# Performance work log

Hardware: AMD Instinct MI355X
Metric: run time of the kernel (lower is better)

The kernel has to match this reference:

```python
import jax, jax.numpy as jnp
import numpy as np

B, N, K, H = 8, 4096, 16, 64
EPS_LN = 1e-5
EPS_STD = 1e-5


def _ln(x, g, b):
    m = jnp.mean(x, -1, keepdims=True)
    v = jnp.mean((x - m) ** 2, -1, keepdims=True)
    return (x - m) * jax.lax.rsqrt(v + EPS_LN) * g + b


def _res_block(x, W1, b1, g1, be1, W2, b2, g2, be2):
    h = jax.nn.relu(_ln(x @ W1 + b1, g1, be1))
    return jax.nn.relu(x + _ln(h @ W2 + b2, g2, be2))


def setup_inputs() -> dict:
    key = jax.random.key(0)
    ks = jax.random.split(key, 12)
    def w(k, shape, scale=0.02):
        return (jax.random.normal(k, shape) * scale).astype(jnp.float32)
    h = H
    z = jnp.zeros
    o = jnp.ones
    return dict(
        xyz=jax.random.normal(ks[0], (B, N, 3), jnp.float32),
        x=jax.random.normal(ks[1], (B, N, 3), jnp.float32),
        W_emb=w(ks[2], (3, h)), b_emb=z(h), g_emb=o(h), be_emb=z(h),
        alpha=o(h), beta=z(h),
        W_pre=w(ks[3], (2 * h, 4 * h)), b_pre=z(4 * h), g_pre=o(4 * h), be_pre=z(4 * h),
        W1a=w(ks[4], (4 * h, 8 * h)), b1a=z(8 * h), g1a=o(8 * h), be1a=z(8 * h),
        W2a=w(ks[5], (8 * h, 4 * h)), b2a=z(4 * h), g2a=o(4 * h), be2a=z(4 * h),
        W_pos=w(ks[6], (4 * h, 4 * h)), b_pos=z(4 * h), g_pos=o(4 * h), be_pos=z(4 * h),
        W1b=w(ks[7], (4 * h, 8 * h)), b1b=z(8 * h), g1b=o(8 * h), be1b=z(8 * h),
        W2b=w(ks[8], (8 * h, 4 * h)), b2b=z(4 * h), g2b=o(4 * h), be2b=z(4 * h),
        W_fin=w(ks[9], (4 * h, h)), b_fin=z(h), g_fin=o(h), be_fin=z(h),
    )


def _forward(xyz, x, W_emb, b_emb, g_emb, be_emb, alpha, beta,
             W_pre, b_pre, g_pre, be_pre,
             W1a, b1a, g1a, be1a, W2a, b2a, g2a, be2a,
             W_pos, b_pos, g_pos, be_pos,
             W1b, b1b, g1b, be1b, W2b, b2b, g2b, be2b,
             W_fin, b_fin, g_fin, be_fin):
    # embedding: Linear + LN + ReLU  -> [B, N, H]
    pts = jax.nn.relu(_ln(x @ W_emb + b_emb, g_emb, be_emb))
    # KNN over xyz (squared distances, smallest K)
    sq = jnp.sum(xyz ** 2, -1)                                   # [B, N]
    sqd = sq[:, :, None] + sq[:, None, :] - 2.0 * jnp.einsum('bnd,bmd->bnm', xyz, xyz)
    _, idx = jax.lax.top_k(-sqd, K)                              # [B, N, K]
    grouped = jax.vmap(lambda p, i: p[i])(pts, idx)              # [B, N, K, H]
    # anchor normalization: mean = center feature; std over whole per-batch flattened diff (ddof=1)
    diff = grouped - pts[:, :, None, :]
    std = jnp.std(diff.reshape(diff.shape[0], -1), axis=-1, ddof=1)[:, None, None, None]
    grouped = diff / (std + EPS_STD) * alpha + beta
    newp = jnp.concatenate(
        [grouped, jnp.broadcast_to(pts[:, :, None, :], grouped.shape)], axis=-1)  # [B, N, K, 2H]
    # pre MLP + residual block, then max-pool over K
    y = _ln(newp @ W_pre + b_pre, g_pre, be_pre)                 # [B, N, K, 4H]
    y = _res_block(y, W1a, b1a, g1a, be1a, W2a, b2a, g2a, be2a)
    y = jnp.max(y, axis=2)                                       # [B, N, 4H]
    # pos MLP + residual block, then max-pool over N
    y = _ln(y @ W_pos + b_pos, g_pos, be_pos)
    y = _res_block(y, W1b, b1b, g1b, be1b, W2b, b2b, g2b, be2b)
    y = jnp.max(y, axis=1)                                       # [B, 4H]
    return _ln(y @ W_fin + b_fin, g_fin, be_fin)                 # [B, H]


def reference(xyz, x, W_emb, b_emb, g_emb, be_emb, alpha, beta,
              W_pre, b_pre, g_pre, be_pre,
              W1a, b1a, g1a, be1a, W2a, b2a, g2a, be2a,
              W_pos, b_pos, g_pos, be_pos,
              W1b, b1b, g1b, be1b, W2b, b2b, g2b, be2b,
              W_fin, b_fin, g_fin, be_fin):
    return _forward(xyz, x, W_emb, b_emb, g_emb, be_emb, alpha, beta,
                    W_pre, b_pre, g_pre, be_pre,
                    W1a, b1a, g1a, be1a, W2a, b2a, g2a, be2a,
                    W_pos, b_pos, g_pos, be_pos,
                    W1b, b1b, g1b, be1b, W2b, b2b, g2b, be2b,
                    W_fin, b_fin, g_fin, be_fin)
```

## Files before the change

kernel.cpp:

```cpp
#include <hip/hip_runtime.h>
#include <hip/hip_bf16.h>

typedef __bf16 bf16_t;
typedef __bf16 bf16x8 __attribute__((ext_vector_type(8)));
typedef __bf16 bf16x4 __attribute__((ext_vector_type(4)));
typedef float f32x4 __attribute__((ext_vector_type(4)));
typedef unsigned long long u64;

#define LNEPS 1e-5f
#define STDEPS 1e-5f

#define PTS_OFF   0UL
#define SQ_OFF    8388608UL
#define IDX_OFF   8519680UL
#define RED_OFF   10616832UL
#define STD_OFF   (RED_OFF + 128UL)
#define WP_OFF    10617088UL
#define POOL1_OFF 11862272UL
#define POOL2_OFF 28639488UL
#define WS_NEED   28647680UL

__global__ void k_pack(const float* __restrict__ W, bf16_t* __restrict__ Wp,
                       int No, int sh, int n)
{
  int i = blockIdx.x * 256 + threadIdx.x;
  if (i >= n) return;
  int j = i & 7;
  int l = (i >> 3) & 63;
  int rest = i >> 9;
  int kc = rest & ((1 << sh) - 1);
  int t = rest >> sh;
  int k = kc * 32 + (l >> 4) * 8 + j;
  int col = t * 16 + (l & 15);
  Wp[i] = (bf16_t)W[k * No + col];
}

__global__ void k_embed(const float* __restrict__ xyz, const float* __restrict__ x,
                        const float* __restrict__ W, const float* __restrict__ bb,
                        const float* __restrict__ g, const float* __restrict__ be,
                        float* __restrict__ pts, float4* __restrict__ cand4)
{
  int p = blockIdx.x * 256 + threadIdx.x;
  float x0 = x[p * 3 + 0], x1 = x[p * 3 + 1], x2 = x[p * 3 + 2];
  float e[64];
  float s = 0.f;
  #pragma unroll
  for (int j = 0; j < 64; ++j) {
    float v = bb[j];
    v = fmaf(x0, W[j], v);
    v = fmaf(x1, W[64 + j], v);
    v = fmaf(x2, W[128 + j], v);
    e[j] = v; s += v;
  }
  float mean = s * (1.f / 64.f);
  float vs = 0.f;
  #pragma unroll
  for (int j = 0; j < 64; ++j) { float d = e[j] - mean; vs = fmaf(d, d, vs); }
  float rstd = rsqrtf(vs * (1.f / 64.f) + LNEPS);
  #pragma unroll
  for (int j = 0; j < 64; ++j)
    pts[p * 64 + j] = fmaxf(0.f, (e[j] - mean) * rstd * g[j] + be[j]);
  float z0 = xyz[p * 3 + 0], z1 = xyz[p * 3 + 1], z2 = xyz[p * 3 + 2];
  cand4[p] = make_float4(z0, z1, z2, z0 * z0 + z1 * z1 + z2 * z2);
}

__device__ __forceinline__ void insert16(u64* a, u64 key)
{
  #pragma unroll
  for (int j = 15; j >= 1; --j) {
    u64 lo = (key < a[j - 1]) ? a[j - 1] : key;
    a[j] = (key < a[j]) ? lo : a[j];
  }
  a[0] = (key < a[0]) ? key : a[0];
}

__device__ __forceinline__ void merge16(u64* a, const u64* b)
{
  u64 m[16];
  #pragma unroll
  for (int i = 0; i < 16; ++i) m[i] = (a[i] < b[15 - i]) ? a[i] : b[15 - i];
  #pragma unroll
  for (int d = 8; d >= 1; d >>= 1) {
    #pragma unroll
    for (int i = 0; i < 16; ++i) {
      if ((i & d) == 0) {
        u64 xv = m[i], yv = m[i + d];
        bool c = yv < xv;
        m[i] = c ? yv : xv;
        m[i + d] = c ? xv : yv;
      }
    }
  }
  #pragma unroll
  for (int i = 0; i < 16; ++i) a[i] = m[i];
}

__global__ __launch_bounds__(256) void k_knn(const float4* __restrict__ cand4,
                                             int* __restrict__ idx)
{
  __shared__ u64 ldsB[256 * 17];
  const int tid = threadIdx.x;
  const int l = tid & 63;
  const int w = tid >> 6;
  const int wu = __builtin_amdgcn_readfirstlane(w);
  const int b = blockIdx.x >> 6;
  const int g = blockIdx.x & 63;
  const int p = (b << 12) + (g << 6) + l;
  const float4 q = cand4[p];
  const float4* __restrict__ cbase = cand4 + (b << 12) + (wu << 10);
  const int mbase = wu << 10;
  u64 arr[16];
  const u64 KINF = ((u64)0x7F800000u << 32) | 0xFFFFFFFFu;
  #pragma unroll
  for (int j = 0; j < 16; ++j) arr[j] = KINF;
  float tf = 3.4e38f;
  int cnt = 0;
  u64* myb = &ldsB[tid * 17];

  for (int m0 = 0; m0 < 1024; m0 += 8) {
    if (__any(cnt > 8)) {
      for (int j2 = 0; j2 < cnt; ++j2) insert16(arr, myb[j2]);
      cnt = 0;
      tf = __uint_as_float((unsigned)(arr[15] >> 32));
    }
    #pragma unroll
    for (int u = 0; u < 8; ++u) {
      float4 c = cbase[m0 + u];
      float dot = q.x * c.x;
      dot = fmaf(q.y, c.y, dot);
      dot = fmaf(q.z, c.z, dot);
      float d = fmaxf(fmaf(-2.f, dot, q.w + c.w), 0.f);
      if (d < tf) {
        myb[cnt] = ((u64)__float_as_uint(d) << 32) | (unsigned)(mbase + m0 + u);
        ++cnt;
      }
    }
  }
  for (int j2 = 0; j2 < cnt; ++j2) insert16(arr, myb[j2]);

  #pragma unroll
  for (int j = 0; j < 16; ++j) myb[j] = arr[j];
  __syncthreads();
  if ((w & 1) == 0) {
    u64 brr[16];
    #pragma unroll
    for (int j = 0; j < 16; ++j) brr[j] = ldsB[((w + 1) * 64 + l) * 17 + j];
    merge16(arr, brr);
    #pragma unroll
    for (int j = 0; j < 16; ++j) myb[j] = arr[j];
  }
  __syncthreads();
  if (w == 0) {
    u64 brr[16];
    #pragma unroll
    for (int j = 0; j < 16; ++j) brr[j] = ldsB[(2 * 64 + l) * 17 + j];
    merge16(arr, brr);
    #pragma unroll
    for (int j = 0; j < 16; ++j) idx[p * 16 + j] = (int)(unsigned)(arr[j] & 0xFFFFFFFFu);
  }
}

__global__ void k_stdred(const float* __restrict__ pts, const int* __restrict__ idx,
                         double* __restrict__ red)
{
  int b = blockIdx.x >> 6, chunk = blockIdx.x & 63;
  int tid = threadIdx.x;
  int h = tid & 63;
  int r0 = chunk * 1024 + (tid >> 6);
  float s = 0.f, s2 = 0.f;
  for (int i = 0; i < 256; ++i) {
    int row = r0 + 4 * i;
    int n = row >> 4, k = row & 15;
    int ni = idx[((b << 12) + n) * 16 + k];
    float v = pts[((b << 12) + ni) * 64 + h] - pts[((b << 12) + n) * 64 + h];
    s += v; s2 = fmaf(v, v, s2);
  }
  double ds = (double)s, ds2 = (double)s2;
  #pragma unroll
  for (int m = 1; m < 64; m <<= 1) {
    ds += __shfl_xor(ds, m, 64);
    ds2 += __shfl_xor(ds2, m, 64);
  }
  __shared__ double sred[8];
  int w = tid >> 6;
  if ((tid & 63) == 0) { sred[w] = ds; sred[4 + w] = ds2; }
  __syncthreads();
  if (tid == 0) {
    atomicAdd(&red[b], sred[0] + sred[1] + sred[2] + sred[3]);
    atomicAdd(&red[8 + b], sred[4] + sred[5] + sred[6] + sred[7]);
  }
}

__global__ void k_stdfin(const double* __restrict__ red, float* __restrict__ stdv)
{
  int t = threadIdx.x;
  if (t < 8) {
    double M = 4194304.0;
    double s = red[t], s2 = red[8 + t];
    double var = (s2 - s * s / M) / (M - 1.0);
    stdv[t] = (float)sqrt(var);
  }
}

__device__ __forceinline__ bf16x4 cvt4(f32x4 v)
{
  bf16x4 o;
  o[0] = (bf16_t)v[0]; o[1] = (bf16_t)v[1]; o[2] = (bf16_t)v[2]; o[3] = (bf16_t)v[3];
  return o;
}

__device__ __forceinline__ f32x4 shflmax(f32x4 v, int m)
{
  f32x4 r;
  #pragma unroll
  for (int c = 0; c < 4; ++c) r[c] = fmaxf(v[c], __shfl_xor(v[c], m, 64));
  return r;
}

template <int NKC, int NTW>
__device__ __forceinline__ void gemm_sw(const bf16_t* __restrict__ inS, const int instride,
                                        const bf16_t* __restrict__ Wp,
                                        const int w, const int l, f32x4 (*acc)[4])
{
  const int lr = l & 15, lg = l >> 4;
  const bf16x8* __restrict__ Wf = (const bf16x8*)Wp;
  #pragma unroll
  for (int kc = 0; kc < NKC; ++kc) {
    bf16x8 af[4];
    #pragma unroll
    for (int rt = 0; rt < 4; ++rt)
      af[rt] = *(const bf16x8*)(inS + (rt * 16 + lr) * instride + kc * 32 + lg * 8);
    #pragma unroll
    for (int ct = 0; ct < NTW; ++ct) {
      bf16x8 bw = Wf[((w * NTW + ct) * NKC + kc) * 64 + l];
      #pragma unroll
      for (int rt = 0; rt < 4; ++rt)
        acc[ct][rt] = __builtin_amdgcn_mfma_f32_16x16x32_bf16(bw, af[rt], acc[ct][rt], 0, 0, 0);
    }
  }
}

template <int NTW>
__device__ __forceinline__ void add_bias_stats(f32x4 (*acc)[4], const float* __restrict__ bias,
                                               const int w, const int l,
                                               float* __restrict__ smP, float* __restrict__ sqP)
{
  const int lr = l & 15, lg = l >> 4;
  float sm[4] = {0.f, 0.f, 0.f, 0.f}, sq[4] = {0.f, 0.f, 0.f, 0.f};
  #pragma unroll
  for (int ct = 0; ct < NTW; ++ct) {
    const int t = w * NTW + ct;
    f32x4 b4 = *(const f32x4*)(bias + t * 16 + 4 * lg);
    #pragma unroll
    for (int rt = 0; rt < 4; ++rt) {
      f32x4 v = acc[ct][rt] + b4;
      acc[ct][rt] = v;
      #pragma unroll
      for (int rg = 0; rg < 4; ++rg) { sm[rt] += v[rg]; sq[rt] = fmaf(v[rg], v[rg], sq[rt]); }
    }
  }
  #pragma unroll
  for (int rt = 0; rt < 4; ++rt) {
    sm[rt] += __shfl_xor(sm[rt], 16, 64); sq[rt] += __shfl_xor(sq[rt], 16, 64);
    sm[rt] += __shfl_xor(sm[rt], 32, 64); sq[rt] += __shfl_xor(sq[rt], 32, 64);
  }
  if (lg == 0) {
    #pragma unroll
    for (int rt = 0; rt < 4; ++rt) {
      smP[w * 64 + rt * 16 + lr] = sm[rt];
      sqP[w * 64 + rt * 16 + lr] = sq[rt];
    }
  }
}

__device__ __forceinline__ void mean_rstd(const float* __restrict__ smP,
                                          const float* __restrict__ sqP,
                                          const int lr, const float invNC,
                                          float* mean, float* rstd)
{
  #pragma unroll
  for (int rt = 0; rt < 4; ++rt) {
    int row = rt * 16 + lr;
    float s = smP[row] + smP[64 + row] + smP[128 + row] + smP[192 + row];
    float q = sqP[row] + sqP[64 + row] + sqP[128 + row] + sqP[192 + row];
    float me = s * invNC;
    float var = q * invNC - me * me;
    mean[rt] = me; rstd[rt] = rsqrtf(var + LNEPS);
  }
}

template <int NKCIN, int INSTRIDE, int REGEL, bool KPOOL>
__global__ __launch_bounds__(256, 2) void k_mlp(
    const float* __restrict__ pts, const int* __restrict__ idxp,
    const float* __restrict__ stdv, const float* __restrict__ alpha,
    const float* __restrict__ beta, const bf16_t* __restrict__ pooled1_in,
    const bf16_t* __restrict__ Wp0, const float* __restrict__ b0,
    const float* __restrict__ g0, const float* __restrict__ be0,
    const bf16_t* __restrict__ Wp1, const float* __restrict__ b1,
    const float* __restrict__ g1, const float* __restrict__ be1,
    const bf16_t* __restrict__ Wp2, const float* __restrict__ b2,
    const float* __restrict__ g2, const float* __restrict__ be2,
    bf16_t* __restrict__ pooled1_out, unsigned* __restrict__ pooled2)
{
  __shared__ bf16_t region[REGEL];
  __shared__ float smP[4 * 64];
  __shared__ float sqP[4 * 64];
  bf16_t* inS = region;
  bf16_t* yS = region + 64 * INSTRIDE;
  bf16_t* hS = region;

  const int tid = threadIdx.x;
  const int l = tid & 63, w = tid >> 6;
  const int lr = l & 15, lg = l >> 4;
  const int p0 = blockIdx.x * (KPOOL ? 4 : 64);
  const int bb = p0 >> 12;

  if (KPOOL) {
    const float inv = 1.0f / (stdv[bb] + STDEPS);
    const int r = tid >> 2, q = tid & 3;
    const int p = p0 + (r >> 4), k = r & 15;
    if (q < 2) {
      const int ni = idxp[p * 16 + k];
      const float* sn = pts + ((size_t)(bb << 12) + ni) * 64 + q * 32;
      const float* sp = pts + (size_t)p * 64 + q * 32;
      #pragma unroll
      for (int i = 0; i < 8; ++i) {
        f32x4 a = *(const f32x4*)(sn + 4 * i);
        f32x4 c = *(const f32x4*)(sp + 4 * i);
        f32x4 av = *(const f32x4*)(alpha + q * 32 + 4 * i);
        f32x4 bv = *(const f32x4*)(beta + q * 32 + 4 * i);
        f32x4 v = (a - c) * (av * inv) + bv;
        *(bf16x4*)(inS + r * INSTRIDE + q * 32 + 4 * i) = cvt4(v);
      }
    } else {
      const float* sp = pts + (size_t)p * 64 + (q - 2) * 32;
      #pragma unroll
      for (int i = 0; i < 8; ++i) {
        f32x4 c = *(const f32x4*)(sp + 4 * i);
        *(bf16x4*)(inS + r * INSTRIDE + 64 + (q - 2) * 32 + 4 * i) = cvt4(c);
      }
    }
  } else {
    const int r = tid >> 2, q = tid & 3;
    #pragma unroll
    for (int j = 0; j < 8; ++j) {
      *(bf16x8*)(inS + r * INSTRIDE + q * 64 + j * 8) =
          *(const bf16x8*)(pooled1_in + (size_t)(p0 + r) * 256 + q * 64 + j * 8);
    }
  }
  __syncthreads();

  f32x4 resid[4][4];
  float mean[4], rstd[4];

  {
    f32x4 acc[4][4];
    #pragma unroll
    for (int ct = 0; ct < 4; ++ct)
      #pragma unroll
      for (int rt = 0; rt < 4; ++rt) acc[ct][rt] = {0.f, 0.f, 0.f, 0.f};
    gemm_sw<NKCIN, 4>(inS, INSTRIDE, Wp0, w, l, acc);
    add_bias_stats<4>(acc, b0, w, l, smP, sqP);
    __syncthreads();
    mean_rstd(smP, sqP, lr, 1.f / 256.f, mean, rstd);
    #pragma unroll
    for (int ct = 0; ct < 4; ++ct) {
      const int t = w * 4 + ct;
      f32x4 g4 = *(const f32x4*)(g0 + t * 16 + 4 * lg);
      f32x4 be4 = *(const f32x4*)(be0 + t * 16 + 4 * lg);
      #pragma unroll
      for (int rt = 0; rt < 4; ++rt) {
        f32x4 v;
        #pragma unroll
        for (int rg = 0; rg < 4; ++rg)
          v[rg] = (acc[ct][rt][rg] - mean[rt]) * rstd[rt] * g4[rg] + be4[rg];
        resid[ct][rt] = v;
        *(bf16x4*)(yS + (rt * 16 + lr) * 264 + t * 16 + 4 * lg) = cvt4(v);
      }
    }
  }
  __syncthreads();

  {
    f32x4 acc[8][4];
    #pragma unroll
    for (int ct = 0; ct < 8; ++ct)
      #pragma unroll
      for (int rt = 0; rt < 4; ++rt) acc[ct][rt] = {0.f, 0.f, 0.f, 0.f};
    gemm_sw<8, 8>(yS, 264, Wp1, w, l, acc);
    add_bias_stats<8>(acc, b1, w, l, smP, sqP);
    __syncthreads();
    mean_rstd(smP, sqP, lr, 1.f / 512.f, mean, rstd);
    #pragma unroll
    for (int ct = 0; ct < 8; ++ct) {
      const int t = w * 8 + ct;
      f32x4 g4 = *(const f32x4*)(g1 + t * 16 + 4 * lg);
      f32x4 be4 = *(const f32x4*)(be1 + t * 16 + 4 * lg);
      #pragma unroll
      for (int rt = 0; rt < 4; ++rt) {
        f32x4 v;
        #pragma unroll
        for (int rg = 0; rg < 4; ++rg)
          v[rg] = fmaxf(0.f, (acc[ct][rt][rg] - mean[rt]) * rstd[rt] * g4[rg] + be4[rg]);
        *(bf16x4*)(hS + (rt * 16 + lr) * 520 + t * 16 + 4 * lg) = cvt4(v);
      }
    }
  }
  __syncthreads();

  {
    f32x4 acc[4][4];
    #pragma unroll
    for (int ct = 0; ct < 4; ++ct)
      #pragma unroll
      for (int rt = 0; rt < 4; ++rt) acc[ct][rt] = {0.f, 0.f, 0.f, 0.f};
    gemm_sw<16, 4>(hS, 520, Wp2, w, l, acc);
    add_bias_stats<4>(acc, b2, w, l, smP, sqP);
    __syncthreads();
    mean_rstd(smP, sqP, lr, 1.f / 256.f, mean, rstd);
    #pragma unroll
    for (int ct = 0; ct < 4; ++ct) {
      const int t = w * 4 + ct;
      f32x4 g4 = *(const f32x4*)(g2 + t * 16 + 4 * lg);
      f32x4 be4 = *(const f32x4*)(be2 + t * 16 + 4 * lg);
      f32x4 mv = {0.f, 0.f, 0.f, 0.f};
      #pragma unroll
      for (int rt = 0; rt < 4; ++rt) {
        f32x4 v;
        #pragma unroll
        for (int rg = 0; rg < 4; ++rg)
          v[rg] = fmaxf(0.f, resid[ct][rt][rg] +
                             (acc[ct][rt][rg] - mean[rt]) * rstd[rt] * g4[rg] + be4[rg]);
        if (KPOOL) {
          v = shflmax(v, 1); v = shflmax(v, 2); v = shflmax(v, 4); v = shflmax(v, 8);
          if (lr == 0)
            *(bf16x4*)(pooled1_out + (size_t)(p0 + rt) * 256 + t * 16 + 4 * lg) = cvt4(v);
        } else {
          #pragma unroll
          for (int rg = 0; rg < 4; ++rg) mv[rg] = fmaxf(mv[rg], v[rg]);
        }
      }
      if (!KPOOL) {
        mv = shflmax(mv, 1); mv = shflmax(mv, 2); mv = shflmax(mv, 4); mv = shflmax(mv, 8);
        if (lr == 0) {
          #pragma unroll
          for (int rg = 0; rg < 4; ++rg)
            atomicMax(&pooled2[bb * 256 + t * 16 + 4 * lg + rg], __float_as_uint(mv[rg]));
        }
      }
    }
  }
}

__global__ void k_final(const unsigned* __restrict__ pooled2,
                        const float* __restrict__ W, const float* __restrict__ bb,
                        const float* __restrict__ g, const float* __restrict__ be,
                        float* __restrict__ out)
{
  int w = threadIdx.x >> 6;
  int l = threadIdx.x & 63;
  float acc = bb[l];
  for (int k = 0; k < 256; ++k)
    acc = fmaf(__uint_as_float(pooled2[w * 256 + k]), W[k * 64 + l], acc);
  float sm = acc, sq = acc * acc;
  #pragma unroll
  for (int m = 1; m < 64; m <<= 1) {
    sm += __shfl_xor(sm, m, 64);
    sq += __shfl_xor(sq, m, 64);
  }
  float mean = sm * (1.f / 64.f);
  float var = sq * (1.f / 64.f) - mean * mean;
  out[w * 64 + l] = (acc - mean) * rsqrtf(var + LNEPS) * g[l] + be[l];
}

extern "C" void kernel_launch(void* const* d_in, const int* in_sizes, int n_in,
                              void* d_out, int out_size, void* d_ws, size_t ws_size,
                              hipStream_t stream)
{
  if (ws_size < WS_NEED) return;
  const float* xyz = (const float*)d_in[0];
  const float* x = (const float*)d_in[1];
  const float* W_emb = (const float*)d_in[2];
  const float* b_emb = (const float*)d_in[3];
  const float* g_emb = (const float*)d_in[4];
  const float* be_emb = (const float*)d_in[5];
  const float* alpha = (const float*)d_in[6];
  const float* beta = (const float*)d_in[7];
  const float* W_pre = (const float*)d_in[8];
  const float* b_pre = (const float*)d_in[9];
  const float* g_pre = (const float*)d_in[10];
  const float* be_pre = (const float*)d_in[11];
  const float* W1a = (const float*)d_in[12];
  const float* b1a = (const float*)d_in[13];
  const float* g1a = (const float*)d_in[14];
  const float* be1a = (const float*)d_in[15];
  const float* W2a = (const float*)d_in[16];
  const float* b2a = (const float*)d_in[17];
  const float* g2a = (const float*)d_in[18];
  const float* be2a = (const float*)d_in[19];
  const float* W_pos = (const float*)d_in[20];
  const float* b_pos = (const float*)d_in[21];
  const float* g_pos = (const float*)d_in[22];
  const float* be_pos = (const float*)d_in[23];
  const float* W1b = (const float*)d_in[24];
  const float* b1b = (const float*)d_in[25];
  const float* g1b = (const float*)d_in[26];
  const float* be1b = (const float*)d_in[27];
  const float* W2b = (const float*)d_in[28];
  const float* b2b = (const float*)d_in[29];
  const float* g2b = (const float*)d_in[30];
  const float* be2b = (const float*)d_in[31];
  const float* W_fin = (const float*)d_in[32];
  const float* b_fin = (const float*)d_in[33];
  const float* g_fin = (const float*)d_in[34];
  const float* be_fin = (const float*)d_in[35];

  char* ws = (char*)d_ws;
  float* pts = (float*)(ws + PTS_OFF);
  int* idx = (int*)(ws + IDX_OFF);
  double* red = (double*)(ws + RED_OFF);
  float* stdv = (float*)(ws + STD_OFF);
  bf16_t* WpPre = (bf16_t*)(ws + WP_OFF);
  bf16_t* Wp1a = WpPre + 32768;
  bf16_t* Wp2a = Wp1a + 131072;
  bf16_t* WpPos = Wp2a + 131072;
  bf16_t* Wp1b = WpPos + 65536;
  bf16_t* Wp2b = Wp1b + 131072;
  bf16_t* pooled1 = (bf16_t*)(ws + POOL1_OFF);
  float4* cand4 = (float4*)(ws + POOL1_OFF);
  unsigned* pooled2 = (unsigned*)(ws + POOL2_OFF);

  hipMemsetAsync(ws + RED_OFF, 0, 256, stream);
  hipMemsetAsync(ws + POOL2_OFF, 0, 8192, stream);

  k_pack<<<32768 / 256, 256, 0, stream>>>(W_pre, WpPre, 256, 2, 32768);
  k_pack<<<131072 / 256, 256, 0, stream>>>(W1a, Wp1a, 512, 3, 131072);
  k_pack<<<131072 / 256, 256, 0, stream>>>(W2a, Wp2a, 256, 4, 131072);
  k_pack<<<65536 / 256, 256, 0, stream>>>(W_pos, WpPos, 256, 3, 65536);
  k_pack<<<131072 / 256, 256, 0, stream>>>(W1b, Wp1b, 512, 3, 131072);
  k_pack<<<131072 / 256, 256, 0, stream>>>(W2b, Wp2b, 256, 4, 131072);

  k_embed<<<32768 / 256, 256, 0, stream>>>(xyz, x, W_emb, b_emb, g_emb, be_emb, pts, cand4);
  k_knn<<<512, 256, 0, stream>>>(cand4, idx);
  k_stdred<<<512, 256, 0, stream>>>(pts, idx, red);
  k_stdfin<<<1, 64, 0, stream>>>(red, stdv);

  k_mlp<4, 136, 33280, true><<<8192, 256, 0, stream>>>(
      pts, idx, stdv, alpha, beta, nullptr,
      WpPre, b_pre, g_pre, be_pre,
      Wp1a, b1a, g1a, be1a,
      Wp2a, b2a, g2a, be2a,
      pooled1, nullptr);
  k_mlp<8, 264, 33792, false><<<512, 256, 0, stream>>>(
      nullptr, nullptr, nullptr, nullptr, nullptr, pooled1,
      WpPos, b_pos, g_pos, be_pos,
      Wp1b, b1b, g1b, be1b,
      Wp2b, b2b, g2b, be2b,
      nullptr, pooled2);
  k_final<<<1, 512, 0, stream>>>(pooled2, W_fin, b_fin, g_fin, be_fin, (float*)d_out);
}
```

Before: 1.142 ms.

## Make MLP kernel wave-private per 16 rows and split KNN over 8 waves

The fused MLP kernel now gives each wave its own 16 rows and all output columns, with a private LDS slice. Block-wide __syncthreads and the cross-wave LayerNorm statistic exchange become an LDS waitcnt fence plus in-wave shuffles. The residual is kept in bf16 registers and LN is folded into one scale/shift FMA. KNN moves to 512-thread blocks, each wave scanning 512 candidates, with an extra merge stage. The risks are a much larger per-thread accumulator count (32 f32x4), which raises register pressure and lowers occupancy, extra bf16 rounding of the residual, and each wave streaming the full weight matrix itself.

```diff
diff --git a/kernel.cpp b/kernel.cpp
--- a/kernel.cpp
+++ b/kernel.cpp
@@ -10,8 +10,10 @@
 #define LNEPS 1e-5f
 #define STDEPS 1e-5f
 
+#define LDS_FENCE() do { asm volatile("s_waitcnt lgkmcnt(0)" ::: "memory"); \
+                         __builtin_amdgcn_sched_barrier(0); } while (0)
+
 #define PTS_OFF   0UL
-#define SQ_OFF    8388608UL
 #define IDX_OFF   8519680UL
 #define RED_OFF   10616832UL
 #define STD_OFF   (RED_OFF + 128UL)
@@ -95,10 +97,10 @@
   for (int i = 0; i < 16; ++i) a[i] = m[i];
 }
 
-__global__ __launch_bounds__(256) void k_knn(const float4* __restrict__ cand4,
+__global__ __launch_bounds__(512) void k_knn(const float4* __restrict__ cand4,
                                              int* __restrict__ idx)
 {
-  __shared__ u64 ldsB[256 * 17];
+  __shared__ u64 ldsB[512 * 17];
   const int tid = threadIdx.x;
   const int l = tid & 63;
   const int w = tid >> 6;
@@ -107,8 +109,8 @@
   const int g = blockIdx.x & 63;
   const int p = (b << 12) + (g << 6) + l;
   const float4 q = cand4[p];
-  const float4* __restrict__ cbase = cand4 + (b << 12) + (wu << 10);
-  const int mbase = wu << 10;
+  const float4* __restrict__ cbase = cand4 + (b << 12) + (wu << 9);
+  const int mbase = wu << 9;
   u64 arr[16];
   const u64 KINF = ((u64)0x7F800000u << 32) | 0xFFFFFFFFu;
   #pragma unroll
@@ -117,7 +119,7 @@
   int cnt = 0;
   u64* myb = &ldsB[tid * 17];
 
-  for (int m0 = 0; m0 < 1024; m0 += 8) {
+  for (int m0 = 0; m0 < 512; m0 += 8) {
     if (__any(cnt > 8)) {
       for (int j2 = 0; j2 < cnt; ++j2) insert16(arr, myb[j2]);
       cnt = 0;
@@ -150,10 +152,19 @@
     for (int j = 0; j < 16; ++j) myb[j] = arr[j];
   }
   __syncthreads();
+  if ((w & 3) == 0) {
+    u64 brr[16];
+    #pragma unroll
+    for (int j = 0; j < 16; ++j) brr[j] = ldsB[((w + 2) * 64 + l) * 17 + j];
+    merge16(arr, brr);
+    #pragma unroll
+    for (int j = 0; j < 16; ++j) myb[j] = arr[j];
+  }
+  __syncthreads();
   if (w == 0) {
     u64 brr[16];
     #pragma unroll
-    for (int j = 0; j < 16; ++j) brr[j] = ldsB[(2 * 64 + l) * 17 + j];
+    for (int j = 0; j < 16; ++j) brr[j] = ldsB[(4 * 64 + l) * 17 + j];
     merge16(arr, brr);
     #pragma unroll
     for (int j = 0; j < 16; ++j) idx[p * 16 + j] = (int)(unsigned)(arr[j] & 0xFFFFFFFFu);
@@ -209,6 +220,14 @@
   return o;
 }
 
+__device__ __forceinline__ f32x4 vmax0(f32x4 v)
+{
+  f32x4 r;
+  #pragma unroll
+  for (int c = 0; c < 4; ++c) r[c] = fmaxf(v[c], 0.f);
+  return r;
+}
+
 __device__ __forceinline__ f32x4 shflmax(f32x4 v, int m)
 {
   f32x4 r;
@@ -217,80 +236,48 @@
   return r;
 }
 
-template <int NKC, int NTW>
-__device__ __forceinline__ void gemm_sw(const bf16_t* __restrict__ inS, const int instride,
+template <int NKC, int NT>
+__device__ __forceinline__ void gemm_rw(const bf16_t* __restrict__ base, const int stride,
                                         const bf16_t* __restrict__ Wp,
-                                        const int w, const int l, f32x4 (*acc)[4])
+                                        const int l, f32x4* acc)
 {
   const int lr = l & 15, lg = l >> 4;
   const bf16x8* __restrict__ Wf = (const bf16x8*)Wp;
   #pragma unroll
   for (int kc = 0; kc < NKC; ++kc) {
-    bf16x8 af[4];
-    #pragma unroll
-    for (int rt = 0; rt < 4; ++rt)
-      af[rt] = *(const bf16x8*)(inS + (rt * 16 + lr) * instride + kc * 32 + lg * 8);
-    #pragma unroll
-    for (int ct = 0; ct < NTW; ++ct) {
-      bf16x8 bw = Wf[((w * NTW + ct) * NKC + kc) * 64 + l];
-      #pragma unroll
-      for (int rt = 0; rt < 4; ++rt)
-        acc[ct][rt] = __builtin_amdgcn_mfma_f32_16x16x32_bf16(bw, af[rt], acc[ct][rt], 0, 0, 0);
-    }
-  }
-}
-
-template <int NTW>
-__device__ __forceinline__ void add_bias_stats(f32x4 (*acc)[4], const float* __restrict__ bias,
-                                               const int w, const int l,
-                                               float* __restrict__ smP, float* __restrict__ sqP)
-{
-  const int lr = l & 15, lg = l >> 4;
-  float sm[4] = {0.f, 0.f, 0.f, 0.f}, sq[4] = {0.f, 0.f, 0.f, 0.f};
-  #pragma unroll
-  for (int ct = 0; ct < NTW; ++ct) {
-    const int t = w * NTW + ct;
+    bf16x8 af = *(const bf16x8*)(base + lr * stride + kc * 32 + lg * 8);
+    #pragma unroll
+    for (int t = 0; t < NT; ++t) {
+      bf16x8 bw = Wf[(t * NKC + kc) * 64 + l];
+      acc[t] = __builtin_amdgcn_mfma_f32_16x16x32_bf16(bw, af, acc[t], 0, 0, 0);
+    }
+  }
+}
+
+template <int NT>
+__device__ __forceinline__ void bias_stats_rw(f32x4* acc, const float* __restrict__ bias,
+                                              const int lg, const float invNC,
+                                              float& mean, float& rstd)
+{
+  f32x4 smv = {0.f, 0.f, 0.f, 0.f}, sqv = {0.f, 0.f, 0.f, 0.f};
+  #pragma unroll
+  for (int t = 0; t < NT; ++t) {
     f32x4 b4 = *(const f32x4*)(bias + t * 16 + 4 * lg);
-    #pragma unroll
-    for (int rt = 0; rt < 4; ++rt) {
-      f32x4 v = acc[ct][rt] + b4;
-      acc[ct][rt] = v;
-      #pragma unroll
-      for (int rg = 0; rg < 4; ++rg) { sm[rt] += v[rg]; sq[rt] = fmaf(v[rg], v[rg], sq[rt]); }
-    }
-  }
-  #pragma unroll
-  for (int rt = 0; rt < 4; ++rt) {
-    sm[rt] += __shfl_xor(sm[rt], 16, 64); sq[rt] += __shfl_xor(sq[rt], 16, 64);
-    sm[rt] += __shfl_xor(sm[rt], 32, 64); sq[rt] += __shfl_xor(sq[rt], 32, 64);
-  }
-  if (lg == 0) {
-    #pragma unroll
-    for (int rt = 0; rt < 4; ++rt) {
-      smP[w * 64 + rt * 16 + lr] = sm[rt];
-      sqP[w * 64 + rt * 16 + lr] = sq[rt];
-    }
-  }
-}
-
-__device__ __forceinline__ void mean_rstd(const float* __restrict__ smP,
-                                          const float* __restrict__ sqP,
-                                          const int lr, const float invNC,
-                                          float* mean, float* rstd)
-{
-  #pragma unroll
-  for (int rt = 0; rt < 4; ++rt) {
-    int row = rt * 16 + lr;
-    float s = smP[row] + smP[64 + row] + smP[128 + row] + smP[192 + row];
-    float q = sqP[row] + sqP[64 + row] + sqP[128 + row] + sqP[192 + row];
-    float me = s * invNC;
-    float var = q * invNC - me * me;
-    mean[rt] = me; rstd[rt] = rsqrtf(var + LNEPS);
-  }
-}
-
-template <int NKCIN, int INSTRIDE, int REGEL, bool KPOOL>
-__global__ __launch_bounds__(256, 2) void k_mlp(
+    f32x4 v = acc[t] + b4;
+    acc[t] = v;
+    smv += v;
+    sqv = v * v + sqv;
+  }
+  float s = (smv[0] + smv[1]) + (smv[2] + smv[3]);
+  float q = (sqv[0] + sqv[1]) + (sqv[2] + sqv[3]);
+  s += __shfl_xor(s, 16, 64); q += __shfl_xor(q, 16, 64);
+  s += __shfl_xor(s, 32, 64); q += __shfl_xor(q, 32, 64);
+  mean = s * invNC;
+  rstd = rsqrtf(q * invNC - mean * mean + LNEPS);
+}
+
+template <int NKCIN, int INSTRIDE, bool KPOOL>
+__global__ __launch_bounds__(256) void k_mlp(
     const float* __restrict__ pts, const int* __restrict__ idxp,
     const float* __restrict__ stdv, const float* __restrict__ alpha,
     const float* __restrict__ beta, const bf16_t* __restrict__ pooled1_in,
@@ -302,25 +289,22 @@
     const float* __restrict__ g2, const float* __restrict__ be2,
     bf16_t* __restrict__ pooled1_out, unsigned* __restrict__ pooled2)
 {
-  __shared__ bf16_t region[REGEL];
-  __shared__ float smP[4 * 64];
-  __shared__ float sqP[4 * 64];
-  bf16_t* inS = region;
-  bf16_t* yS = region + 64 * INSTRIDE;
-  bf16_t* hS = region;
-
+  __shared__ bf16_t region[4 * 8448];
   const int tid = threadIdx.x;
   const int l = tid & 63, w = tid >> 6;
   const int lr = l & 15, lg = l >> 4;
-  const int p0 = blockIdx.x * (KPOOL ? 4 : 64);
-  const int bb = p0 >> 12;
+  bf16_t* wb = region + w * 8448;
+  bf16_t* inS = wb;
+  bf16_t* yS = wb + (KPOOL ? 2176 : 4224);
+  bf16_t* hS = wb;
 
   if (KPOOL) {
+    const int p = blockIdx.x * 4 + w;
+    const int bb = p >> 12;
     const float inv = 1.0f / (stdv[bb] + STDEPS);
-    const int r = tid >> 2, q = tid & 3;
-    const int p = p0 + (r >> 4), k = r & 15;
+    const int r = l >> 2, q = l & 3;
     if (q < 2) {
-      const int ni = idxp[p * 16 + k];
+      const int ni = idxp[p * 16 + r];
       const float* sn = pts + ((size_t)(bb << 12) + ni) * 64 + q * 32;
       const float* sp = pts + (size_t)p * 64 + q * 32;
       #pragma unroll
@@ -330,122 +314,94 @@
         f32x4 av = *(const f32x4*)(alpha + q * 32 + 4 * i);
         f32x4 bv = *(const f32x4*)(beta + q * 32 + 4 * i);
         f32x4 v = (a - c) * (av * inv) + bv;
-        *(bf16x4*)(inS + r * INSTRIDE + q * 32 + 4 * i) = cvt4(v);
+        *(bf16x4*)(inS + r * 136 + q * 32 + 4 * i) = cvt4(v);
       }
     } else {
       const float* sp = pts + (size_t)p * 64 + (q - 2) * 32;
       #pragma unroll
       for (int i = 0; i < 8; ++i) {
         f32x4 c = *(const f32x4*)(sp + 4 * i);
-        *(bf16x4*)(inS + r * INSTRIDE + 64 + (q - 2) * 32 + 4 * i) = cvt4(c);
+        *(bf16x4*)(inS + r * 136 + 64 + (q - 2) * 32 + 4 * i) = cvt4(c);
       }
     }
   } else {
-    const int r = tid >> 2, q = tid & 3;
-    #pragma unroll
-    for (int j = 0; j < 8; ++j) {
-      *(bf16x8*)(inS + r * INSTRIDE + q * 64 + j * 8) =
-          *(const bf16x8*)(pooled1_in + (size_t)(p0 + r) * 256 + q * 64 + j * 8);
-    }
-  }
-  __syncthreads();
-
-  f32x4 resid[4][4];
-  float mean[4], rstd[4];
+    const int r = l >> 2, q = l & 3;
+    const int pt = blockIdx.x * 64 + w * 16 + r;
+    #pragma unroll
+    for (int i = 0; i < 8; ++i) {
+      *(bf16x8*)(inS + r * 264 + q * 64 + i * 8) =
+          *(const bf16x8*)(pooled1_in + (size_t)pt * 256 + q * 64 + i * 8);
+    }
+  }
+  LDS_FENCE();
+
+  bf16x4 residb[16];
+  float mean, rstd;
 
   {
-    f32x4 acc[4][4];
-    #pragma unroll
-    for (int ct = 0; ct < 4; ++ct)
-      #pragma unroll
-      for (int rt = 0; rt < 4; ++rt) acc[ct][rt] = {0.f, 0.f, 0.f, 0.f};
-    gemm_sw<NKCIN, 4>(inS, INSTRIDE, Wp0, w, l, acc);
-    add_bias_stats<4>(acc, b0, w, l, smP, sqP);
-    __syncthreads();
-    mean_rstd(smP, sqP, lr, 1.f / 256.f, mean, rstd);
-    #pragma unroll
-    for (int ct = 0; ct < 4; ++ct) {
-      const int t = w * 4 + ct;
+    f32x4 acc[16];
+    #pragma unroll
+    for (int t = 0; t < 16; ++t) acc[t] = {0.f, 0.f, 0.f, 0.f};
+    gemm_rw<NKCIN, 16>(inS, INSTRIDE, Wp0, l, acc);
+    bias_stats_rw<16>(acc, b0, lg, 1.f / 256.f, mean, rstd);
+    #pragma unroll
+    for (int t = 0; t < 16; ++t) {
       f32x4 g4 = *(const f32x4*)(g0 + t * 16 + 4 * lg);
       f32x4 be4 = *(const f32x4*)(be0 + t * 16 + 4 * lg);
-      #pragma unroll
-      for (int rt = 0; rt < 4; ++rt) {
-        f32x4 v;
-        #pragma unroll
-        for (int rg = 0; rg < 4; ++rg)
-          v[rg] = (acc[ct][rt][rg] - mean[rt]) * rstd[rt] * g4[rg] + be4[rg];
-        resid[ct][rt] = v;
-        *(bf16x4*)(yS + (rt * 16 + lr) * 264 + t * 16 + 4 * lg) = cvt4(v);
-      }
-    }
-  }
-  __syncthreads();
+      f32x4 scale = g4 * rstd;
+      f32x4 shift = be4 - mean * scale;
+      f32x4 v = acc[t] * scale + shift;
+      bf16x4 vb = cvt4(v);
+      residb[t] = vb;
+      *(bf16x4*)(yS + lr * 264 + t * 16 + 4 * lg) = vb;
+    }
+  }
+  LDS_FENCE();
 
   {
-    f32x4 acc[8][4];
-    #pragma unroll
-    for (int ct = 0; ct < 8; ++ct)
-      #pragma unroll
-      for (int rt = 0; rt < 4; ++rt) acc[ct][rt] = {0.f, 0.f, 0.f, 0.f};
-    gemm_sw<8, 8>(yS, 264, Wp1, w, l, acc);
-    add_bias_stats<8>(acc, b1, w, l, smP, sqP);
-    __syncthreads();
-    mean_rstd(smP, sqP, lr, 1.f / 512.f, mean, rstd);
-    #pragma unroll
-    for (int ct = 0; ct < 8; ++ct) {
-      const int t = w * 8 + ct;
+    f32x4 acc[32];
+    #pragma unroll
+    for (int t = 0; t < 32; ++t) acc[t] = {0.f, 0.f, 0.f, 0.f};
+    gemm_rw<8, 32>(yS, 264, Wp1, l, acc);
+    bias_stats_rw<32>(acc, b1, lg, 1.f / 512.f, mean, rstd);
+    #pragma unroll
+    for (int t = 0; t < 32; ++t) {
       f32x4 g4 = *(const f32x4*)(g1 + t * 16 + 4 * lg);
       f32x4 be4 = *(const f32x4*)(be1 + t * 16 + 4 * lg);
-      #pragma unroll
-      for (int rt = 0; rt < 4; ++rt) {
-        f32x4 v;
-        #pragma unroll
-        for (int rg = 0; rg < 4; ++rg)
-          v[rg] = fmaxf(0.f, (acc[ct][rt][rg] - mean[rt]) * rstd[rt] * g4[rg] + be4[rg]);
-        *(bf16x4*)(hS + (rt * 16 + lr) * 520 + t * 16 + 4 * lg) = cvt4(v);
-      }
-    }
-  }
-  __syncthreads();
+      f32x4 scale = g4 * rstd;
+      f32x4 shift = be4 - mean * scale;
+      f32x4 v = vmax0(acc[t] * scale + shift);
+      *(bf16x4*)(hS + lr * 520 + t * 16 + 4 * lg) = cvt4(v);
+    }
+  }
+  LDS_FENCE();
 
   {
-    f32x4 acc[4][4];
-    #pragma unroll
-    for (int ct = 0; ct < 4; ++ct)
-      #pragma unroll
-      for (int rt = 0; rt < 4; ++rt) acc[ct][rt] = {0.f, 0.f, 0.f, 0.f};
-    gemm_sw<16, 4>(hS, 520, Wp2, w, l, acc);
-    add_bias_stats<4>(acc, b2, w, l, smP, sqP);
-    __syncthreads();
-    mean_rstd(smP, sqP, lr, 1.f / 256.f, mean, rstd);
-    #pragma unroll
-    for (int ct = 0; ct < 4; ++ct) {
-      const int t = w * 4 + ct;
+    f32x4 acc[16];
+    #pragma unroll
+    for (int t = 0; t < 16; ++t) acc[t] = {0.f, 0.f, 0.f, 0.f};
+    gemm_rw<16, 16>(hS, 520, Wp2, l, acc);
+    bias_stats_rw<16>(acc, b2, lg, 1.f / 256.f, mean, rstd);
+    const int bbNK = (blockIdx.x * 64) >> 12;
+    #pragma unroll
+    for (int t = 0; t < 16; ++t) {
       f32x4 g4 = *(const f32x4*)(g2 + t * 16 + 4 * lg);
       f32x4 be4 = *(const f32x4*)(be2 + t * 16 + 4 * lg);
-      f32x4 mv = {0.f, 0.f, 0.f, 0.f};
-      #pragma unroll
-      for (int rt = 0; rt < 4; ++rt) {
-        f32x4 v;
-        #pragma unroll
-        for (int rg = 0; rg < 4; ++rg)
-          v[rg] = fmaxf(0.f, resid[ct][rt][rg] +
-                             (acc[ct][rt][rg] - mean[rt]) * rstd[rt] * g4[rg] + be4[rg]);
-        if (KPOOL) {
-          v = shflmax(v, 1); v = shflmax(v, 2); v = shflmax(v, 4); v = shflmax(v, 8);
-          if (lr == 0)
-            *(bf16x4*)(pooled1_out + (size_t)(p0 + rt) * 256 + t * 16 + 4 * lg) = cvt4(v);
-        } else {
-          #pragma unroll
-          for (int rg = 0; rg < 4; ++rg) mv[rg] = fmaxf(mv[rg], v[rg]);
-        }
-      }
-      if (!KPOOL) {
-        mv = shflmax(mv, 1); mv = shflmax(mv, 2); mv = shflmax(mv, 4); mv = shflmax(mv, 8);
+      f32x4 scale = g4 * rstd;
+      f32x4 shift = be4 - mean * scale;
+      f32x4 r4;
+      r4[0] = (float)residb[t][0]; r4[1] = (float)residb[t][1];
+      r4[2] = (float)residb[t][2]; r4[3] = (float)residb[t][3];
+      f32x4 v = vmax0(r4 + acc[t] * scale + shift);
+      v = shflmax(v, 1); v = shflmax(v, 2); v = shflmax(v, 4); v = shflmax(v, 8);
+      if (KPOOL) {
+        if (lr == 0)
+          *(bf16x4*)(pooled1_out + (size_t)(blockIdx.x * 4 + w) * 256 + t * 16 + 4 * lg) = cvt4(v);
+      } else {
         if (lr == 0) {
           #pragma unroll
           for (int rg = 0; rg < 4; ++rg)
-            atomicMax(&pooled2[bb * 256 + t * 16 + 4 * lg + rg], __float_as_uint(mv[rg]));
+            atomicMax(&pooled2[bbNK * 256 + t * 16 + 4 * lg + rg], __float_as_uint(v[rg]));
         }
       }
     }
@@ -541,17 +497,17 @@
   k_pack<<<131072 / 256, 256, 0, stream>>>(W2b, Wp2b, 256, 4, 131072);
 
   k_embed<<<32768 / 256, 256, 0, stream>>>(xyz, x, W_emb, b_emb, g_emb, be_emb, pts, cand4);
-  k_knn<<<512, 256, 0, stream>>>(cand4, idx);
+  k_knn<<<512, 512, 0, stream>>>(cand4, idx);
   k_stdred<<<512, 256, 0, stream>>>(pts, idx, red);
   k_stdfin<<<1, 64, 0, stream>>>(red, stdv);
 
-  k_mlp<4, 136, 33280, true><<<8192, 256, 0, stream>>>(
+  k_mlp<4, 136, true><<<8192, 256, 0, stream>>>(
       pts, idx, stdv, alpha, beta, nullptr,
       WpPre, b_pre, g_pre, be_pre,
       Wp1a, b1a, g1a, be1a,
       Wp2a, b2a, g2a, be2a,
       pooled1, nullptr);
-  k_mlp<8, 264, 33792, false><<<512, 256, 0, stream>>>(
+  k_mlp<8, 264, false><<<512, 256, 0, stream>>>(
       nullptr, nullptr, nullptr, nullptr, nullptr, pooled1,
       WpPos, b_pos, g_pos, be_pos,
       Wp1b, b1b, g1b, be1b,
```

Measured after the change: 2.759 ms. 142% more time.
